# Optimization experiments

Hardware: AMD Instinct MI355X
Metric: run time of the kernel (lower is better)

The kernel has to match this reference:

```python
import jax, jax.numpy as jnp
import numpy as np

U = 50000
I = 50000
N = U + I
D = 128
T = 3
L = 2
E = 3200000
B = 4096


def setup_inputs() -> dict:
    key = jax.random.key(0)
    ks = jax.random.split(key, 20)
    xav = lambda k, shp: jax.random.normal(k, shp, jnp.float32) * (2.0 / (shp[0] + shp[-1])) ** 0.5
    return {
        'user_indices': jax.random.randint(ks[0], (B,), 0, U, jnp.int32),
        'item_indices': jax.random.randint(ks[1], (B,), 0, I, jnp.int32),
        'edge_index': jax.random.randint(ks[2], (2, E), 0, N, jnp.int32),
        'adj_values': jax.random.uniform(ks[3], (E,), jnp.float32),
        'user_table': jax.random.normal(ks[4], (U, D), jnp.float32) * 0.01,
        'item_table': jax.random.normal(ks[5], (I, D), jnp.float32) * 0.01,
        'temporal_emb': xav(ks[6], (T, D)),
        'gcn_w': jnp.stack([xav(ks[7 + l], (D, D)) for l in range(L)]),
        'gcn_b': jnp.zeros((L, D), jnp.float32),
        'att_w1': xav(ks[9], (2 * D, D)), 'att_b1': jnp.zeros((D,), jnp.float32),
        'att_w2': xav(ks[10], (D, T)), 'att_b2': jnp.zeros((T,), jnp.float32),
        'pred_w1': xav(ks[11], (2 * D, D)), 'pred_b1': jnp.zeros((D,), jnp.float32),
        'pred_w2': xav(ks[12], (D, 1)), 'pred_b2': jnp.zeros((1,), jnp.float32),
    }


def _spmm(edge_index, adj_values, s):
    # A @ s with COO adjacency: gather src rows, scale, scatter-add to dst rows
    msgs = adj_values[:, None] * s[edge_index[1]]  # [E, D]
    return jax.ops.segment_sum(msgs, edge_index[0], num_segments=N)


def reference(user_indices, item_indices, edge_index, adj_values, user_table,
              item_table, temporal_emb, gcn_w, gcn_b, att_w1, att_b1, att_w2,
              att_b2, pred_w1, pred_b1, pred_w2, pred_b2):
    user_emb = user_table[user_indices]          # [B, D]
    item_emb = item_table[item_indices]          # [B, D]
    x = jnp.concatenate([user_table, item_table], axis=0)  # [N, D]

    temporal_outs = []
    for t in range(T):
        h = x + temporal_emb[t]
        for l in range(L):
            support = h @ gcn_w[l]
            h = jax.nn.relu(_spmm(edge_index, adj_values, support) + gcn_b[l])
        bu = h[:U][user_indices]                 # [B, D]
        bi = h[U:][item_indices]                 # [B, D]
        temporal_outs.append(jnp.concatenate([bu, bi], axis=1))
    temporal_stack = jnp.stack(temporal_outs, axis=1)  # [B, T, 2D]

    concat_orig = jnp.concatenate([user_emb, item_emb], axis=1)  # [B, 2D]
    att_h = jax.nn.relu(concat_orig @ att_w1 + att_b1)
    attn = jax.nn.softmax(att_h @ att_w2 + att_b2, axis=1)       # [B, T]
    summed = jnp.sum(temporal_stack * attn[:, :, None], axis=1)  # [B, 2D]

    ph = jax.nn.relu(summed @ pred_w1 + pred_b1)  # dropout in eval mode: identity
    pred = ph @ pred_w2 + pred_b2                 # [B, 1]
    return pred.squeeze(-1)
```

## Files before the change

### kernel.cpp

```cpp
#include <hip/hip_runtime.h>

#define U_CNT 50000
#define I_CNT 50000
#define N_NODES 100000
#define DD 128
#define T_STEPS 3
#define E_CNT 3200000
#define B_SZ 4096

#define NCOARSE 391
#define NBLK_BIN 256
#define CHUNK ((E_CNT + NBLK_BIN - 1) / NBLK_BIN)
#define SORT_CAP 10240
#define S_SCALE 256.0f
#define S_INV (1.0f / 256.0f)
#define VQ 32767.0f
#define VQ_INV (1.0f / 32767.0f)
#define FB 8

typedef float v2f __attribute__((ext_vector_type(2)));
typedef short bf16x8 __attribute__((ext_vector_type(8)));
typedef float f32x4 __attribute__((ext_vector_type(4)));

#define CVT4(s, sel) __builtin_amdgcn_cvt_scalef32_pk_f32_fp4((s), 1.0f, (sel))

__device__ __forceinline__ float bf2f(unsigned short u) {
    return __uint_as_float(((unsigned int)u) << 16);
}
__device__ __forceinline__ unsigned short f2bf(float f) {
    unsigned int x = __float_as_uint(f);
    x += 0x7FFF + ((x >> 16) & 1);
    return (unsigned short)(x >> 16);
}

__global__ void __launch_bounds__(256) k_bin_count(const int* __restrict__ dst,
                                                   int* __restrict__ histT) {
    __shared__ int c[NCOARSE];
    int blk = blockIdx.x, tid = threadIdx.x;
    for (int j = tid; j < NCOARSE; j += 256) c[j] = 0;
    __syncthreads();
    int s0 = blk * CHUNK, s1 = min(E_CNT, s0 + CHUNK);
    for (int i = s0 + tid; i < s1; i += 256)
        atomicAdd(&c[__builtin_nontemporal_load(&dst[i]) >> 8], 1);
    __syncthreads();
    for (int j = tid; j < NCOARSE; j += 256) histT[j * NBLK_BIN + blk] = c[j];
}

__global__ void __launch_bounds__(NBLK_BIN) k_scan_bT(int* __restrict__ histT,
                                                      int* __restrict__ tot) {
    __shared__ int lds[NBLK_BIN];
    int b = blockIdx.x, tid = threadIdx.x;
    int v = histT[b * NBLK_BIN + tid];
    lds[tid] = v;
    __syncthreads();
    for (int off = 1; off < NBLK_BIN; off <<= 1) {
        int add = (tid >= off) ? lds[tid - off] : 0;
        __syncthreads();
        lds[tid] += add;
        __syncthreads();
    }
    histT[b * NBLK_BIN + tid] = lds[tid] - v;
    if (tid == NBLK_BIN - 1) tot[b] = lds[tid];
}

__global__ void k_scan_a2(const int* __restrict__ tot, int* __restrict__ exact_base,
                          int* __restrict__ row_ptr) {
    if (threadIdx.x == 0 && blockIdx.x == 0) {
        int run = 0;
        for (int b = 0; b < NCOARSE; ++b) {
            exact_base[b] = run;
            run += tot[b];
        }
        exact_base[NCOARSE] = run;
        row_ptr[N_NODES] = run;
    }
}

__global__ void __launch_bounds__(256) k_bin_scatter(const int* __restrict__ dst,
                                                     const int* __restrict__ src,
                                                     const float* __restrict__ val,
                                                     const int* __restrict__ histT,
                                                     const int* __restrict__ exact_base,
                                                     int2* __restrict__ binned) {
    __shared__ int cur[NCOARSE];
    int blk = blockIdx.x, tid = threadIdx.x;
    for (int b = tid; b < NCOARSE; b += 256)
        cur[b] = exact_base[b] + histT[b * NBLK_BIN + blk];
    __syncthreads();
    int s0 = blk * CHUNK, s1 = min(E_CNT, s0 + CHUNK);
    for (int i = s0 + tid; i < s1; i += 256) {
        int d = __builtin_nontemporal_load(&dst[i]);
        int s = __builtin_nontemporal_load(&src[i]);
        float w = __builtin_nontemporal_load(&val[i]);
        int b = d >> 8;
        int pos = atomicAdd(&cur[b], 1);
        binned[pos] = make_int2(s | ((d & 255) << 20), __float_as_int(w));
    }
}

__global__ void __launch_bounds__(256) k_sort(const int* __restrict__ exact_base,
                                              const int2* __restrict__ binned,
                                              unsigned int* __restrict__ outp,
                                              int* __restrict__ row_ptr) {
    __shared__ int hist[256], scn[256], cur[256];
    __shared__ unsigned short perm[SORT_CAP];
    int b = blockIdx.x, tid = threadIdx.x;
    int ebase = exact_base[b];
    int cnt = exact_base[b + 1] - ebase;
    if (cnt > SORT_CAP) cnt = SORT_CAP;
    const int2* rbase = binned + ebase;
    int n0 = b << 8;
    hist[tid] = 0;
    __syncthreads();
    for (int i = tid; i < cnt; i += 256) atomicAdd(&hist[(rbase[i].x >> 20) & 255], 1);
    __syncthreads();
    scn[tid] = hist[tid];
    __syncthreads();
    for (int off = 1; off < 256; off <<= 1) {
        int v = (tid >= off) ? scn[tid - off] : 0;
        __syncthreads();
        scn[tid] += v;
        __syncthreads();
    }
    int excl = scn[tid] - hist[tid];
    cur[tid] = excl;
    if (n0 + tid < N_NODES) row_ptr[n0 + tid] = ebase + excl;
    __syncthreads();
    for (int i = tid; i < cnt; i += 256) {
        int dloc = (rbase[i].x >> 20) & 255;
        int pos = atomicAdd(&cur[dloc], 1);
        perm[pos] = (unsigned short)i;
    }
    __syncthreads();
    for (int i = tid; i < cnt; i += 256) {
        int2 p = rbase[perm[i]];
        unsigned vq = (unsigned)(__int_as_float(p.y) * VQ + 0.5f);
        outp[ebase + i] = (vq << 17) | (unsigned)(p.x & 0x1FFFF);
    }
}

__global__ void k_uvec(const float* __restrict__ temb, const float* __restrict__ w0,
                       float* __restrict__ u) {
    int k = threadIdx.x;
    for (int t = 0; t < T_STEPS; ++t) {
        float acc = 0.f;
        for (int j = 0; j < DD; ++j) acc += temb[t * DD + j] * w0[j * DD + k];
        u[t * DD + k] = acc;
    }
}

__global__ void __launch_bounds__(256) k_gemm0(const float* __restrict__ utab,
                                               const float* __restrict__ itab,
                                               const float* __restrict__ W,
                                               unsigned char* __restrict__ outf4) {
    __shared__ unsigned short wfrag[8][4][64][8];
    __shared__ unsigned short xs[64 * 128];
    int tid = threadIdx.x;
    #pragma unroll
    for (int ii = 0; ii < 16; ++ii) {
        int idx = tid * 64 + ii * 4;
        int k = idx >> 7, n0 = idx & 127;
        float4 w4 = *reinterpret_cast<const float4*>(&W[idx]);
        int s = k >> 5, kb = (k >> 3) & 3, j = k & 7;
        float wv[4] = {w4.x, w4.y, w4.z, w4.w};
        #pragma unroll
        for (int m = 0; m < 4; ++m) {
            int n = n0 + m;
            wfrag[n >> 4][s][(n & 15) | (kb << 4)][j] = f2bf(wv[m]);
        }
    }
    int lane = tid & 63, wid = tid >> 6;
    const int ntiles = (N_NODES + 63) / 64;
    for (int tile = blockIdx.x; tile < ntiles; tile += gridDim.x) {
        __syncthreads();
        int tbase = tile * 64;
        #pragma unroll
        for (int p = 0; p < 8; ++p) {
            int idx = p * 1024 + tid * 4;
            int row = idx >> 7, c = idx & 127;
            int grow = tbase + row;
            float4 a = make_float4(0.f, 0.f, 0.f, 0.f);
            if (grow < N_NODES) {
                const float* src = (grow < U_CNT) ? &utab[(size_t)grow * DD + c]
                                                  : &itab[(size_t)(grow - U_CNT) * DD + c];
                a = *reinterpret_cast<const float4*>(src);
            }
            int si = (row * 128 + c) ^ ((row & 7) << 3);
            ushort4 o = {f2bf(a.x), f2bf(a.y), f2bf(a.z), f2bf(a.w)};
            *reinterpret_cast<ushort4*>(&xs[si]) = o;
        }
        __syncthreads();
        int rowt = wid * 16 + (lane & 15);
        int kb = lane >> 4;
        bf16x8 afrag[4];
        #pragma unroll
        for (int s = 0; s < 4; ++s) {
            int si = (rowt * 128 + s * 32 + kb * 8) ^ ((rowt & 7) << 3);
            afrag[s] = *reinterpret_cast<bf16x8*>(&xs[si]);
        }
        int wbase = tbase + wid * 16;
        f32x4 accs[8];
        #pragma unroll
        for (int c = 0; c < 8; ++c) {
            f32x4 acc = {0.f, 0.f, 0.f, 0.f};
            #pragma unroll
            for (int s = 0; s < 4; ++s) {
                bf16x8 bfrag = *reinterpret_cast<bf16x8*>(&wfrag[c][s][lane][0]);
                acc = __builtin_amdgcn_mfma_f32_16x16x32_bf16(afrag[s], bfrag, acc, 0, 0, 0);
            }
            accs[c] = acc;
        }
        int l16 = lane & 15;
        int orow0 = wbase + (lane >> 4) * 4;
        #pragma unroll
        for (int c = 0; c < 4; ++c) {
            #pragma unroll
            for (int r = 0; r < 4; ++r) {
                int orow = orow0 + r;
                if (orow < N_NODES) {
                    unsigned byte = __builtin_amdgcn_cvt_scalef32_pk_fp4_f32(
                        0u, accs[c][r] * S_SCALE, accs[c + 4][r] * S_SCALE, 1.0f, 0);
                    outf4[(size_t)orow * 64 + c * 16 + l16] = (unsigned char)(byte & 0xFF);
                }
            }
        }
    }
}

__global__ void __launch_bounds__(256) k_spmm_full(const int* __restrict__ row_ptr,
                                                   const unsigned int* __restrict__ pack,
                                                   const unsigned char* __restrict__ Sf4,
                                                   unsigned short* __restrict__ Pb,
                                                   float* __restrict__ rvec) {
    int wave = (int)((blockIdx.x * blockDim.x + threadIdx.x) >> 6);
    int lane = threadIdx.x & 63;
    if (wave >= N_NODES) return;
    int beg = row_ptr[wave], end = row_ptr[wave + 1];
    int q = lane >> 3;
    int cg = lane & 7;
    v2f acc[8];
    #pragma unroll
    for (int j = 0; j < 8; ++j) acc[j] = (v2f){0.f, 0.f};
    float vs = 0.f;
    int e0 = beg + q;
    unsigned pl0 = (e0 < end) ? __builtin_nontemporal_load(&pack[e0]) : 0u;
    int2 s_cur = make_int2(0, 0);
    if (beg < end)
        s_cur = *reinterpret_cast<const int2*>(&Sf4[((size_t)(pl0 & 0x1FFFF) << 6) + (cg << 3)]);
    float v_cur = (float)(pl0 >> 17) * VQ_INV;
    unsigned pl_next = (e0 + 8 < end) ? __builtin_nontemporal_load(&pack[e0 + 8]) : 0u;
    for (int e = beg; e < end; e += 8) {
        bool more = (e + 8 < end);
        int2 s_next = make_int2(0, 0);
        if (more)
            s_next = *reinterpret_cast<const int2*>(
                &Sf4[((size_t)(pl_next & 0x1FFFF) << 6) + (cg << 3)]);
        float v_n = (float)(pl_next >> 17) * VQ_INV;
        int e2 = e + 16 + q;
        unsigned pl2 = (e2 < end) ? __builtin_nontemporal_load(&pack[e2]) : 0u;
        v2f vv = {v_cur, v_cur};
        acc[0] += vv * CVT4(s_cur.x, 0);
        acc[1] += vv * CVT4(s_cur.x, 1);
        acc[2] += vv * CVT4(s_cur.x, 2);
        acc[3] += vv * CVT4(s_cur.x, 3);
        acc[4] += vv * CVT4(s_cur.y, 0);
        acc[5] += vv * CVT4(s_cur.y, 1);
        acc[6] += vv * CVT4(s_cur.y, 2);
        acc[7] += vv * CVT4(s_cur.y, 3);
        if (cg == 0) vs += v_cur;
        s_cur = s_next;
        v_cur = v_n;
        pl_next = pl2;
    }
    float out[16];
    #pragma unroll
    for (int j = 0; j < 8; ++j) {
        out[j] = acc[j].x;
        out[8 + j] = acc[j].y;
    }
    #pragma unroll
    for (int j = 0; j < 16; ++j) {
        out[j] += __shfl_down(out[j], 32, 64);
        out[j] += __shfl_down(out[j], 16, 64);
        out[j] += __shfl_down(out[j], 8, 64);
        out[j] *= S_INV;
    }
    vs += __shfl_down(vs, 32, 64);
    vs += __shfl_down(vs, 16, 64);
    vs += __shfl_down(vs, 8, 64);
    if (lane < 8) {
        unsigned w0 = ((unsigned)f2bf(out[1]) << 16) | f2bf(out[0]);
        unsigned w1 = ((unsigned)f2bf(out[3]) << 16) | f2bf(out[2]);
        unsigned w2 = ((unsigned)f2bf(out[5]) << 16) | f2bf(out[4]);
        unsigned w3 = ((unsigned)f2bf(out[7]) << 16) | f2bf(out[6]);
        unsigned w4 = ((unsigned)f2bf(out[9]) << 16) | f2bf(out[8]);
        unsigned w5 = ((unsigned)f2bf(out[11]) << 16) | f2bf(out[10]);
        unsigned w6 = ((unsigned)f2bf(out[13]) << 16) | f2bf(out[12]);
        unsigned w7 = ((unsigned)f2bf(out[15]) << 16) | f2bf(out[14]);
        unsigned short* base0 = &Pb[((size_t)wave << 7) + (lane << 3)];
        *reinterpret_cast<int4*>(base0) = make_int4(w0, w1, w2, w3);
        *reinterpret_cast<int4*>(base0 + 64) = make_int4(w4, w5, w6, w7);
        if (lane == 0) rvec[wave] = vs;
    }
}

__global__ void __launch_bounds__(256) k_spmm_out3(const int* __restrict__ row_ptr,
                                                   const unsigned int* __restrict__ pack,
                                                   const unsigned short* __restrict__ Pb,
                                                   const float* __restrict__ rvec,
                                                   const int* __restrict__ uidx,
                                                   const int* __restrict__ iidx,
                                                   const float* __restrict__ uvec,
                                                   const float* __restrict__ b0,
                                                   float* __restrict__ agg) {
    int slot = (int)((blockIdx.x * blockDim.x + threadIdx.x) >> 6);
    int lane = threadIdx.x & 63;
    if (slot >= 2 * B_SZ) return;
    int b = slot & (B_SZ - 1), side = slot >> 12;
    int row = side ? (U_CNT + iidx[b]) : uidx[b];
    int beg = row_ptr[row], end = row_ptr[row + 1];
    int half = lane >> 5, cg = lane & 31;
    float u0[4], u1[4], u2[4], bb[4];
    #pragma unroll
    for (int j = 0; j < 4; ++j) {
        int c = cg * 4 + j;
        u0[j] = uvec[c];
        u1[j] = uvec[DD + c];
        u2[j] = uvec[2 * DD + c];
        bb[j] = b0[c];
    }
    float a0[4] = {0, 0, 0, 0}, a1[4] = {0, 0, 0, 0}, a2[4] = {0, 0, 0, 0};
    for (int e = beg; e < end; e += 2) {
        int ee = e + half;
        unsigned pw = (ee < end) ? __builtin_nontemporal_load(&pack[ee]) : 0u;
        int sx = (int)(pw & 0x1FFFF);
        float v = (float)(pw >> 17) * VQ_INV;
        float rr = rvec[sx];
        ushort4 s4 = *reinterpret_cast<const ushort4*>(&Pb[(size_t)sx * DD + cg * 4]);
        float pc[4] = {bf2f(s4.x), bf2f(s4.y), bf2f(s4.z), bf2f(s4.w)};
        #pragma unroll
        for (int j = 0; j < 4; ++j) {
            float base = pc[j] + bb[j];
            a0[j] += v * fmaxf(base + rr * u0[j], 0.f);
            a1[j] += v * fmaxf(base + rr * u1[j], 0.f);
            a2[j] += v * fmaxf(base + rr * u2[j], 0.f);
        }
    }
    #pragma unroll
    for (int j = 0; j < 4; ++j) {
        a0[j] += __shfl_down(a0[j], 32, 64);
        a1[j] += __shfl_down(a1[j], 32, 64);
        a2[j] += __shfl_down(a2[j], 32, 64);
    }
    if (lane < 32) {
        size_t rb = (size_t)slot * 3;
        float4 o0 = {a0[0], a0[1], a0[2], a0[3]};
        float4 o1 = {a1[0], a1[1], a1[2], a1[3]};
        float4 o2 = {a2[0], a2[1], a2[2], a2[3]};
        *reinterpret_cast<float4*>(&agg[(rb + 0) * DD + lane * 4]) = o0;
        *reinterpret_cast<float4*>(&agg[(rb + 1) * DD + lane * 4]) = o1;
        *reinterpret_cast<float4*>(&agg[(rb + 2) * DD + lane * 4]) = o2;
    }
}

__global__ void __launch_bounds__(256) k_head(const float* __restrict__ agg,
                                              const float* __restrict__ W,
                                              const float* __restrict__ b1,
                                              float* __restrict__ tstack) {
    __shared__ unsigned short wfrag[8][4][64][8];
    __shared__ unsigned short xs[64 * 128];
    __shared__ float blds[DD];
    int tid = threadIdx.x;
    #pragma unroll
    for (int ii = 0; ii < 16; ++ii) {
        int idx = tid * 64 + ii * 4;
        int k = idx >> 7, n0 = idx & 127;
        float4 w4 = *reinterpret_cast<const float4*>(&W[idx]);
        int s = k >> 5, kb = (k >> 3) & 3, j = k & 7;
        float wv[4] = {w4.x, w4.y, w4.z, w4.w};
        #pragma unroll
        for (int m = 0; m < 4; ++m) {
            int n = n0 + m;
            wfrag[n >> 4][s][(n & 15) | (kb << 4)][j] = f2bf(wv[m]);
        }
    }
    if (tid < DD) blds[tid] = b1[tid];
    int lane = tid & 63, wid = tid >> 6;
    const int NR = 2 * B_SZ * T_STEPS;
    const int ntiles = NR / 64;
    for (int tile = blockIdx.x; tile < ntiles; tile += gridDim.x) {
        __syncthreads();
        int tbase = tile * 64;
        #pragma unroll
        for (int p = 0; p < 8; ++p) {
            int idx = p * 1024 + tid * 4;
            int row = idx >> 7, c = idx & 127;
            float4 a = *reinterpret_cast<const float4*>(&agg[(size_t)(tbase + row) * DD + c]);
            int si = (row * 128 + c) ^ ((row & 7) << 3);
            ushort4 o = {f2bf(a.x), f2bf(a.y), f2bf(a.z), f2bf(a.w)};
            *reinterpret_cast<ushort4*>(&xs[si]) = o;
        }
        __syncthreads();
        int rowt = wid * 16 + (lane & 15);
        int kb = lane >> 4;
        bf16x8 afrag[4];
        #pragma unroll
        for (int s = 0; s < 4; ++s) {
            int si = (rowt * 128 + s * 32 + kb * 8) ^ ((rowt & 7) << 3);
            afrag[s] = *reinterpret_cast<bf16x8*>(&xs[si]);
        }
        int wbase = tbase + wid * 16;
        #pragma unroll
        for (int c = 0; c < 8; ++c) {
            f32x4 acc = {0.f, 0.f, 0.f, 0.f};
            #pragma unroll
            for (int s = 0; s < 4; ++s) {
                bf16x8 bfrag = *reinterpret_cast<bf16x8*>(&wfrag[c][s][lane][0]);
                acc = __builtin_amdgcn_mfma_f32_16x16x32_bf16(afrag[s], bfrag, acc, 0, 0, 0);
            }
            int orow0 = wbase + (lane >> 4) * 4;
            int ocol = c * 16 + (lane & 15);
            float bb = blds[ocol];
            #pragma unroll
            for (int r = 0; r < 4; ++r) {
                int orow = orow0 + r;
                int slot = orow / 3, t = orow - slot * 3;
                int bi = slot & (B_SZ - 1), side = slot >> 12;
                float o = fmaxf(acc[r] + bb, 0.f);
                tstack[((size_t)bi * T_STEPS + t) * 2 * DD + side * DD + ocol] = o;
            }
        }
    }
}

__global__ void __launch_bounds__(256) k_final(const int* __restrict__ uidx,
                                               const int* __restrict__ iidx,
                                               const float* __restrict__ utab,
                                               const float* __restrict__ itab,
                                               const float* __restrict__ aw1,
                                               const float* __restrict__ ab1,
                                               const float* __restrict__ aw2,
                                               const float* __restrict__ ab2,
                                               const float* __restrict__ pw1,
                                               const float* __restrict__ pb1,
                                               const float* __restrict__ pw2,
                                               const float* __restrict__ pb2,
                                               const float* __restrict__ tstack,
                                               float* __restrict__ outp) {
    __shared__ float s[FB][2 * DD];
    __shared__ float ah[FB][DD];
    __shared__ float attn[FB][4];
    __shared__ float summed[FB][2 * DD];
    __shared__ float red[FB][DD];
    __shared__ int uu[FB], ii[FB];
    int b0 = blockIdx.x * FB, tid = threadIdx.x;
    if (tid < FB) {
        uu[tid] = uidx[b0 + tid];
        ii[tid] = iidx[b0 + tid];
    }
    __syncthreads();
    #pragma unroll
    for (int r = 0; r < FB; ++r)
        s[r][tid] = (tid < DD) ? utab[(size_t)uu[r] * DD + tid]
                               : itab[(size_t)ii[r] * DD + (tid - DD)];
    __syncthreads();
    {
        int c = tid & 127, g = tid >> 7;
        float acc0 = ab1[c], acc1 = acc0, acc2 = acc0, acc3 = acc0;
        for (int k = 0; k < 2 * DD; ++k) {
            float w = aw1[k * DD + c];
            acc0 += s[g][k] * w;
            acc1 += s[g + 2][k] * w;
            acc2 += s[g + 4][k] * w;
            acc3 += s[g + 6][k] * w;
        }
        ah[g][c] = fmaxf(acc0, 0.f);
        ah[g + 2][c] = fmaxf(acc1, 0.f);
        ah[g + 4][c] = fmaxf(acc2, 0.f);
        ah[g + 6][c] = fmaxf(acc3, 0.f);
    }
    __syncthreads();
    if (tid < FB * T_STEPS) {
        int r = tid / 3, t = tid - r * 3;
        float lg = ab2[t];
        for (int k = 0; k < DD; ++k) lg += ah[r][k] * aw2[k * T_STEPS + t];
        attn[r][t] = lg;
    }
    __syncthreads();
    if (tid < FB) {
        float m = fmaxf(attn[tid][0], fmaxf(attn[tid][1], attn[tid][2]));
        float e0 = expf(attn[tid][0] - m), e1 = expf(attn[tid][1] - m),
              e2 = expf(attn[tid][2] - m);
        float inv = 1.f / (e0 + e1 + e2);
        attn[tid][0] = e0 * inv;
        attn[tid][1] = e1 * inv;
        attn[tid][2] = e2 * inv;
    }
    __syncthreads();
    #pragma unroll
    for (int r = 0; r < FB; ++r) {
        const float* tb = &tstack[(size_t)(b0 + r) * T_STEPS * 2 * DD];
        summed[r][tid] =
            attn[r][0] * tb[tid] + attn[r][1] * tb[2 * DD + tid] + attn[r][2] * tb[4 * DD + tid];
    }
    __syncthreads();
    {
        int c = tid & 127, g = tid >> 7;
        float p0 = pb1[c], p1 = p0, p2 = p0, p3 = p0;
        for (int k = 0; k < 2 * DD; ++k) {
            float w = pw1[k * DD + c];
            p0 += summed[g][k] * w;
            p1 += summed[g + 2][k] * w;
            p2 += summed[g + 4][k] * w;
            p3 += summed[g + 6][k] * w;
        }
        float wc = pw2[c];
        red[g][c] = fmaxf(p0, 0.f) * wc;
        red[g + 2][c] = fmaxf(p1, 0.f) * wc;
        red[g + 4][c] = fmaxf(p2, 0.f) * wc;
        red[g + 6][c] = fmaxf(p3, 0.f) * wc;
    }
    __syncthreads();
    if (tid < FB) {
        float sum = pb2[0];
        for (int k = 0; k < DD; ++k) sum += red[tid][k];
        outp[b0 + tid] = sum;
    }
}

extern "C" void kernel_launch(void* const* d_in, const int* in_sizes, int n_in,
                              void* d_out, int out_size, void* d_ws, size_t ws_size,
                              hipStream_t stream) {
    const int* uidx = (const int*)d_in[0];
    const int* iidx = (const int*)d_in[1];
    const int* eidx = (const int*)d_in[2];
    const float* adj = (const float*)d_in[3];
    const float* utab = (const float*)d_in[4];
    const float* itab = (const float*)d_in[5];
    const float* temb = (const float*)d_in[6];
    const float* gw = (const float*)d_in[7];
    const float* gb = (const float*)d_in[8];
    const float* aw1 = (const float*)d_in[9];
    const float* ab1 = (const float*)d_in[10];
    const float* aw2 = (const float*)d_in[11];
    const float* ab2 = (const float*)d_in[12];
    const float* pw1 = (const float*)d_in[13];
    const float* pb1 = (const float*)d_in[14];
    const float* pw2 = (const float*)d_in[15];
    const float* pb2 = (const float*)d_in[16];

    char* ws = (char*)d_ws;
    size_t off = 0;
    auto alloc = [&](size_t bytes) {
        void* p = ws + off;
        off += (bytes + 255) & ~(size_t)255;
        return p;
    };
    int* histT = (int*)alloc((size_t)NBLK_BIN * NCOARSE * 4);
    int* tot = (int*)alloc((NCOARSE + 1) * 4);
    int* exact_base = (int*)alloc((NCOARSE + 1) * 4);
    int* row_ptr = (int*)alloc((size_t)(N_NODES + 1) * 4);
    unsigned int* sorted = (unsigned int*)alloc((size_t)E_CNT * 4);
    float* rvec = (float*)alloc((size_t)N_NODES * 4);
    float* uvec = (float*)alloc((size_t)T_STEPS * DD * 4);
    void* un = alloc((size_t)E_CNT * 8);
    int2* binned = (int2*)un;
    unsigned char* Sf4 = (unsigned char*)un;
    unsigned short* Pb = (unsigned short*)alloc((size_t)N_NODES * DD * 2);
    float* agg = (float*)alloc((size_t)2 * B_SZ * T_STEPS * DD * 4);
    float* tstack = (float*)alloc((size_t)B_SZ * T_STEPS * 2 * DD * 4);

    k_bin_count<<<NBLK_BIN, 256, 0, stream>>>(eidx, histT);
    k_scan_bT<<<NCOARSE, NBLK_BIN, 0, stream>>>(histT, tot);
    k_scan_a2<<<1, 64, 0, stream>>>(tot, exact_base, row_ptr);
    k_bin_scatter<<<NBLK_BIN, 256, 0, stream>>>(eidx, eidx + E_CNT, adj, histT,
                                                exact_base, binned);
    k_sort<<<NCOARSE, 256, 0, stream>>>(exact_base, binned, sorted, row_ptr);
    k_gemm0<<<512, 256, 0, stream>>>(utab, itab, gw, Sf4);
    k_uvec<<<1, DD, 0, stream>>>(temb, gw, uvec);
    k_spmm_full<<<(N_NODES + 3) / 4, 256, 0, stream>>>(row_ptr, sorted, Sf4, Pb, rvec);
    k_spmm_out3<<<(2 * B_SZ * 64) / 256, 256, 0, stream>>>(row_ptr, sorted, Pb, rvec,
                                                           uidx, iidx, uvec, gb, agg);
    k_head<<<384, 256, 0, stream>>>(agg, gw + DD * DD, gb + DD, tstack);
    k_final<<<B_SZ / FB, 256, 0, stream>>>(uidx, iidx, utab, itab, aw1, ab1, aw2, ab2,
                                           pw1, pb1, pw2, pb2, tstack, (float*)d_out);
}
```

Measured before the change: 288.3 us.

## Split binned edges into packed word plus byte, scatter directly in sort

The bin-scatter kernel now quantizes the edge weight and packs it with the source index into one 32-bit word, storing the local destination row in a separate byte array instead of an 8-byte int2. The sort kernel drops its shared-memory permutation and second pass, writing each packed word straight to its final position through the shared atomic cursor. This cuts intermediate edge traffic from 8 to 5 bytes per edge and removes the SORT_CAP clamp, at the cost of uncoalesced scattered global writes in the sort. The gemm0 grid is also raised from 512 to 768 blocks.

New measurement: 325.4 us. +12.9%, slower.

```diff
diff --git a/kernel.cpp b/kernel.cpp
--- a/kernel.cpp
+++ b/kernel.cpp
@@ -11,7 +11,6 @@
 #define NCOARSE 391
 #define NBLK_BIN 256
 #define CHUNK ((E_CNT + NBLK_BIN - 1) / NBLK_BIN)
-#define SORT_CAP 10240
 #define S_SCALE 256.0f
 #define S_INV (1.0f / 256.0f)
 #define VQ 32767.0f
@@ -81,7 +80,8 @@
                                                      const float* __restrict__ val,
                                                      const int* __restrict__ histT,
                                                      const int* __restrict__ exact_base,
-                                                     int2* __restrict__ binned) {
+                                                     unsigned int* __restrict__ pack4,
+                                                     unsigned char* __restrict__ dloc8) {
     __shared__ int cur[NCOARSE];
     int blk = blockIdx.x, tid = threadIdx.x;
     for (int b = tid; b < NCOARSE; b += 256)
@@ -94,25 +94,25 @@
         float w = __builtin_nontemporal_load(&val[i]);
         int b = d >> 8;
         int pos = atomicAdd(&cur[b], 1);
-        binned[pos] = make_int2(s | ((d & 255) << 20), __float_as_int(w));
+        unsigned vq = (unsigned)(w * VQ + 0.5f);
+        pack4[pos] = (vq << 17) | (unsigned)s;
+        dloc8[pos] = (unsigned char)(d & 255);
     }
 }
 
 __global__ void __launch_bounds__(256) k_sort(const int* __restrict__ exact_base,
-                                              const int2* __restrict__ binned,
+                                              const unsigned int* __restrict__ pack4,
+                                              const unsigned char* __restrict__ dloc8,
                                               unsigned int* __restrict__ outp,
                                               int* __restrict__ row_ptr) {
     __shared__ int hist[256], scn[256], cur[256];
-    __shared__ unsigned short perm[SORT_CAP];
     int b = blockIdx.x, tid = threadIdx.x;
     int ebase = exact_base[b];
     int cnt = exact_base[b + 1] - ebase;
-    if (cnt > SORT_CAP) cnt = SORT_CAP;
-    const int2* rbase = binned + ebase;
     int n0 = b << 8;
     hist[tid] = 0;
     __syncthreads();
-    for (int i = tid; i < cnt; i += 256) atomicAdd(&hist[(rbase[i].x >> 20) & 255], 1);
+    for (int i = tid; i < cnt; i += 256) atomicAdd(&hist[dloc8[ebase + i]], 1);
     __syncthreads();
     scn[tid] = hist[tid];
     __syncthreads();
@@ -127,15 +127,9 @@
     if (n0 + tid < N_NODES) row_ptr[n0 + tid] = ebase + excl;
     __syncthreads();
     for (int i = tid; i < cnt; i += 256) {
-        int dloc = (rbase[i].x >> 20) & 255;
+        int dloc = dloc8[ebase + i];
         int pos = atomicAdd(&cur[dloc], 1);
-        perm[pos] = (unsigned short)i;
-    }
-    __syncthreads();
-    for (int i = tid; i < cnt; i += 256) {
-        int2 p = rbase[perm[i]];
-        unsigned vq = (unsigned)(__int_as_float(p.y) * VQ + 0.5f);
-        outp[ebase + i] = (vq << 17) | (unsigned)(p.x & 0x1FFFF);
+        outp[ebase + pos] = pack4[ebase + i];
     }
 }
 
@@ -563,9 +557,10 @@
     unsigned int* sorted = (unsigned int*)alloc((size_t)E_CNT * 4);
     float* rvec = (float*)alloc((size_t)N_NODES * 4);
     float* uvec = (float*)alloc((size_t)T_STEPS * DD * 4);
-    void* un = alloc((size_t)E_CNT * 8);
-    int2* binned = (int2*)un;
+    void* un = alloc((size_t)E_CNT * 4);
+    unsigned int* pack4 = (unsigned int*)un;
     unsigned char* Sf4 = (unsigned char*)un;
+    unsigned char* dloc8 = (unsigned char*)alloc((size_t)E_CNT);
     unsigned short* Pb = (unsigned short*)alloc((size_t)N_NODES * DD * 2);
     float* agg = (float*)alloc((size_t)2 * B_SZ * T_STEPS * DD * 4);
     float* tstack = (float*)alloc((size_t)B_SZ * T_STEPS * 2 * DD * 4);
@@ -574,9 +569,9 @@
     k_scan_bT<<<NCOARSE, NBLK_BIN, 0, stream>>>(histT, tot);
     k_scan_a2<<<1, 64, 0, stream>>>(tot, exact_base, row_ptr);
     k_bin_scatter<<<NBLK_BIN, 256, 0, stream>>>(eidx, eidx + E_CNT, adj, histT,
-                                                exact_base, binned);
-    k_sort<<<NCOARSE, 256, 0, stream>>>(exact_base, binned, sorted, row_ptr);
-    k_gemm0<<<512, 256, 0, stream>>>(utab, itab, gw, Sf4);
+                                                exact_base, pack4, dloc8);
+    k_sort<<<NCOARSE, 256, 0, stream>>>(exact_base, pack4, dloc8, sorted, row_ptr);
+    k_gemm0<<<768, 256, 0, stream>>>(utab, itab, gw, Sf4);
     k_uvec<<<1, DD, 0, stream>>>(temb, gw, uvec);
     k_spmm_full<<<(N_NODES + 3) / 4, 256, 0, stream>>>(row_ptr, sorted, Sf4, Pb, rvec);
     k_spmm_out3<<<(2 * B_SZ * 64) / 256, 256, 0, stream>>>(row_ptr, sorted, Pb, rvec,
```
